# Kernel optimization log

Hardware: AMD Instinct MI355X
Metric: run time of the kernel (lower is better)

Reference implementation:

```python
import jax, jax.numpy as jnp
import numpy as np

N_HEAD, MODEL_DIM, KEY_DIM, VALUE_DIM = 16, 1024, 64, 64
B, S = 4, 2048
EPS = 1e-5
TEMP = float(np.sqrt(KEY_DIM))


def setup_inputs() -> dict:
    key = jax.random.key(0)
    ks = jax.random.split(key, 12)
    d = {
        'query': jax.random.normal(ks[0], (B, S, MODEL_DIM), jnp.float32),
        'key':   jax.random.normal(ks[1], (B, S, MODEL_DIM), jnp.float32),
        'value': jax.random.normal(ks[2], (B, S, MODEL_DIM), jnp.float32),
        # projection weights stored as [in, out]
        'Wq': jax.random.normal(ks[3], (MODEL_DIM, N_HEAD * KEY_DIM), jnp.float32) * np.sqrt(2.0 / (MODEL_DIM + KEY_DIM)),
        'bq': jnp.zeros((N_HEAD * KEY_DIM,), jnp.float32),
        'Wk': jax.random.normal(ks[4], (MODEL_DIM, N_HEAD * KEY_DIM), jnp.float32) * np.sqrt(2.0 / (MODEL_DIM + KEY_DIM)),
        'bk': jnp.zeros((N_HEAD * KEY_DIM,), jnp.float32),
        'Wv': jax.random.normal(ks[5], (MODEL_DIM, N_HEAD * VALUE_DIM), jnp.float32) * np.sqrt(2.0 / (MODEL_DIM + VALUE_DIM)),
        'bv': jnp.zeros((N_HEAD * VALUE_DIM,), jnp.float32),
        'Wo': jax.random.normal(ks[6], (N_HEAD * VALUE_DIM, MODEL_DIM), jnp.float32) * np.sqrt(2.0 / (N_HEAD * VALUE_DIM + MODEL_DIM)),
        'bo': jnp.zeros((MODEL_DIM,), jnp.float32),
        'ln_gamma': jnp.ones((MODEL_DIM,), jnp.float32),
        'ln_beta': jnp.zeros((MODEL_DIM,), jnp.float32),
    }
    return d


def reference(query, key, value, Wq, bq, Wk, bk, Wv, bv, Wo, bo, ln_gamma, ln_beta):
    b, sq, _ = query.shape
    residual = query
    # QKV projections -> [B, S, H, D]
    q = (query @ Wq + bq).reshape(b, sq, N_HEAD, KEY_DIM)
    k = (key @ Wk + bk).reshape(b, key.shape[1], N_HEAD, KEY_DIM)
    v = (value @ Wv + bv).reshape(b, value.shape[1], N_HEAD, VALUE_DIM)
    # scaled dot-product attention (dropout inactive in eval)
    scores = jnp.einsum('bqhd,bkhd->bhqk', q, k) / TEMP
    attn = jax.nn.softmax(scores, axis=-1)
    out = jnp.einsum('bhqk,bkhd->bqhd', attn, v).reshape(b, sq, N_HEAD * VALUE_DIM)
    # output projection + residual + LayerNorm
    out = out @ Wo + bo + residual
    mu = jnp.mean(out, axis=-1, keepdims=True)
    var = jnp.var(out, axis=-1, keepdims=True)
    return (out - mu) * jax.lax.rsqrt(var + EPS) * ln_gamma + ln_beta
```

## Files before the change

### kernel.cpp

```cpp
#include <hip/hip_runtime.h>
#include <math.h>

#define MD 1024
#define NH 16
#define HD 64
#define BATCH 4
#define SEQ 2048

typedef __attribute__((ext_vector_type(8))) short short8;
typedef __attribute__((ext_vector_type(4))) short short4v;
typedef __attribute__((ext_vector_type(4))) float f32x4;
typedef __attribute__((ext_vector_type(2))) unsigned int uint2v;

#define GLOAD16(gp, lp) __builtin_amdgcn_global_load_lds( \
    (const __attribute__((address_space(1))) void*)(gp),  \
    (__attribute__((address_space(3))) void*)(lp), 16, 0, 0)

__device__ inline unsigned short f2b(float f) {
    unsigned u = __builtin_bit_cast(unsigned, f);
    unsigned r = (u + 0x7fffu + ((u >> 16) & 1u)) >> 16;
    return (unsigned short)r;
}
__device__ inline float b2f(unsigned short s) {
    return __builtin_bit_cast(float, ((unsigned)s) << 16);
}

__global__ __launch_bounds__(256)
void prep_kernel(const float* __restrict__ x0, const float* __restrict__ x1,
                 const float* __restrict__ x2, unsigned short* __restrict__ y0,
                 unsigned short* __restrict__ y1, unsigned short* __restrict__ y2,
                 int n,
                 const float* __restrict__ W0, const float* __restrict__ W1,
                 const float* __restrict__ W2, const float* __restrict__ W3,
                 unsigned short* __restrict__ T0, unsigned short* __restrict__ T1,
                 unsigned short* __restrict__ T2, unsigned short* __restrict__ T3)
{
    __shared__ __attribute__((aligned(16))) float T[64][68];
    const int tid = threadIdx.x;
    if (blockIdx.y < 3) {
        const float* x = (blockIdx.y == 0) ? x0 : (blockIdx.y == 1) ? x1 : x2;
        unsigned short* y = (blockIdx.y == 0) ? y0 : (blockIdx.y == 1) ? y1 : y2;
        int i = (blockIdx.x * 256 + tid) * 8;
        if (i >= n) return;
        f32x4 a = *(const f32x4*)(x + i);
        f32x4 b = *(const f32x4*)(x + i + 4);
        short8 o;
        o[0] = (short)f2b(a[0]); o[1] = (short)f2b(a[1]);
        o[2] = (short)f2b(a[2]); o[3] = (short)f2b(a[3]);
        o[4] = (short)f2b(b[0]); o[5] = (short)f2b(b[1]);
        o[6] = (short)f2b(b[2]); o[7] = (short)f2b(b[3]);
        *(short8*)(y + i) = o;
        return;
    }
    const int bx = blockIdx.x;
    if (bx >= 1024) return;
    const int z = bx >> 8, t = bx & 255;
    const int nt = t & 15, kt = t >> 4;
    const float* W = (z == 0) ? W0 : (z == 1) ? W1 : (z == 2) ? W2 : W3;
    unsigned short* WT = (z == 0) ? T0 : (z == 1) ? T1 : (z == 2) ? T2 : T3;
    #pragma unroll
    for (int i = 0; i < 4; ++i) {
        int u = tid + i * 256;
        int row = u >> 4, c4 = u & 15;
        f32x4 v = *(const f32x4*)(W + (size_t)(kt * 64 + row) * MD + nt * 64 + c4 * 4);
        *(f32x4*)&T[row][c4 * 4] = v;
    }
    __syncthreads();
    #pragma unroll
    for (int i = 0; i < 2; ++i) {
        int u = tid + i * 256;
        int nn = u >> 3, c16 = u & 7;
        short8 o;
        #pragma unroll
        for (int j = 0; j < 8; ++j) o[j] = (short)f2b(T[c16 * 8 + j][nn]);
        *(short8*)(WT + (size_t)(nt * 64 + nn) * MD + kt * 64 + c16 * 8) = o;
    }
}

__device__ __forceinline__ void tile_origin(int* obrow, int* obcol)
{
    const int nbx = gridDim.x;
    const int bid = blockIdx.y * nbx + blockIdx.x;
    const int cpx = (nbx * gridDim.y) >> 3;
    const int swz = (bid & 7) * cpx + (bid >> 3);
    *obrow = (swz / nbx) * 128;
    *obcol = (swz % nbx) * 128;
}

__device__ __forceinline__
void gemm_core3(const unsigned short* __restrict__ A,
                const unsigned short* __restrict__ Bt,
                short* As, short* Bs, f32x4 acc[4][4],
                int brow, int bcol)
{
    const int tid = threadIdx.x;
    const int lane = tid & 63;
    const int wave = tid >> 6;
    const int wm = wave >> 1, wn = wave & 1;
    const int l15 = lane & 15, g = lane >> 4;

    #pragma unroll
    for (int m = 0; m < 4; ++m)
        #pragma unroll
        for (int n = 0; n < 4; ++n) acc[m][n] = (f32x4){0.f, 0.f, 0.f, 0.f};

    const int rA = tid >> 2, cA = (tid & 3) * 8;
    const int rB = rA + 64;

    auto stage = [&](int t) {
        const int kb = t << 5;
        short* as = As + (t % 3) * 4096;
        short* bs = Bs + (t % 3) * 4096;
        GLOAD16(A  + (size_t)(brow + rA) * MD + kb + cA, as + tid * 8);
        GLOAD16(A  + (size_t)(brow + rB) * MD + kb + cA, as + (tid + 256) * 8);
        GLOAD16(Bt + (size_t)(bcol + rA) * MD + kb + cA, bs + tid * 8);
        GLOAD16(Bt + (size_t)(bcol + rB) * MD + kb + cA, bs + (tid + 256) * 8);
    };

    stage(0);
    stage(1);

    for (int t = 0; t < 31; ++t) {
        asm volatile("s_waitcnt vmcnt(4)" ::: "memory");
        __builtin_amdgcn_s_barrier();
        __builtin_amdgcn_sched_barrier(0);
        if (t < 30) stage(t + 2);
        const short* as = As + (t % 3) * 4096;
        const short* bs = Bs + (t % 3) * 4096;
        short8 af[4], bf_[4];
        #pragma unroll
        for (int m = 0; m < 4; ++m)
            af[m] = *(const short8*)&as[(wm * 64 + m * 16 + l15) * 32 + g * 8];
        #pragma unroll
        for (int n = 0; n < 4; ++n)
            bf_[n] = *(const short8*)&bs[(wn * 64 + n * 16 + l15) * 32 + g * 8];
        #pragma unroll
        for (int m = 0; m < 4; ++m)
            #pragma unroll
            for (int n = 0; n < 4; ++n)
                acc[m][n] = __builtin_amdgcn_mfma_f32_16x16x32_bf16(af[m], bf_[n], acc[m][n], 0, 0, 0);
    }
    {
        asm volatile("s_waitcnt vmcnt(0)" ::: "memory");
        __builtin_amdgcn_s_barrier();
        __builtin_amdgcn_sched_barrier(0);
        const short* as = As + (31 % 3) * 4096;
        const short* bs = Bs + (31 % 3) * 4096;
        short8 af[4], bf_[4];
        #pragma unroll
        for (int m = 0; m < 4; ++m)
            af[m] = *(const short8*)&as[(wm * 64 + m * 16 + l15) * 32 + g * 8];
        #pragma unroll
        for (int n = 0; n < 4; ++n)
            bf_[n] = *(const short8*)&bs[(wn * 64 + n * 16 + l15) * 32 + g * 8];
        #pragma unroll
        for (int m = 0; m < 4; ++m)
            #pragma unroll
            for (int n = 0; n < 4; ++n)
                acc[m][n] = __builtin_amdgcn_mfma_f32_16x16x32_bf16(af[m], bf_[n], acc[m][n], 0, 0, 0);
    }
}

__global__ __launch_bounds__(256, 2)
void gemm_qkv(const unsigned short* __restrict__ A0, const unsigned short* __restrict__ A1,
              const unsigned short* __restrict__ A2,
              const unsigned short* __restrict__ B0, const unsigned short* __restrict__ B1,
              const unsigned short* __restrict__ B2,
              const float* __restrict__ b0, const float* __restrict__ b1,
              const float* __restrict__ b2,
              unsigned short* __restrict__ Cq, unsigned short* __restrict__ Ck,
              unsigned short* __restrict__ Cvt)
{
    __shared__ __attribute__((aligned(16))) short As[3 * 4096];
    __shared__ __attribute__((aligned(16))) short Bs[3 * 4096];
    const int z = blockIdx.z;
    const unsigned short* A  = (z == 0) ? A0 : (z == 1) ? A1 : A2;
    const unsigned short* Bt = (z == 0) ? B0 : (z == 1) ? B1 : B2;
    const float* bias        = (z == 0) ? b0 : (z == 1) ? b1 : b2;

    int brow, bcol;
    tile_origin(&brow, &bcol);
    f32x4 acc[4][4];
    gemm_core3(A, Bt, As, Bs, acc, brow, bcol);

    const int tid = threadIdx.x;
    const int lane = tid & 63;
    const int wave = tid >> 6;
    const int wm = wave >> 1, wn = wave & 1;
    const int l15 = lane & 15, g = lane >> 4;

    if (z == 2) {
        #pragma unroll
        for (int m = 0; m < 4; ++m) {
            #pragma unroll
            for (int n = 0; n < 4; ++n) {
                const int col = bcol + wn * 64 + n * 16 + l15;
                const int h = col >> 6, d = col & 63;
                const float bv_ = bias[col];
                const int row0 = brow + wm * 64 + m * 16 + 4 * g;
                const int bb = row0 >> 11, s = row0 & 2047;
                short4v pk;
                #pragma unroll
                for (int r = 0; r < 4; ++r) pk[r] = (short)f2b(acc[m][n][r] + bv_);
                *(short4v*)(Cvt + ((size_t)((bb << 4) + h) * 64 + d) * SEQ + s) = pk;
            }
        }
        return;
    }
    const float scale = (z == 0) ? (0.125f * 1.44269504088896f) : 1.0f;
    unsigned short* C = (z == 0) ? Cq : Ck;
    #pragma unroll
    for (int m = 0; m < 4; ++m) {
        #pragma unroll
        for (int n = 0; n < 4; ++n) {
            const int col = bcol + wn * 64 + n * 16 + l15;
            const float bcol_v = bias[col];
            #pragma unroll
            for (int r = 0; r < 4; ++r) {
                const size_t row = (size_t)(brow + wm * 64 + m * 16 + 4 * g + r);
                C[row * MD + col] = f2b((acc[m][n][r] + bcol_v) * scale);
            }
        }
    }
}

__global__ __launch_bounds__(256, 2)
void gemm_o(const unsigned short* __restrict__ A, const unsigned short* __restrict__ Bt,
            const float* __restrict__ bias, const float* __restrict__ residual,
            float* __restrict__ Cf)
{
    __shared__ __attribute__((aligned(16))) short As[3 * 4096];
    __shared__ __attribute__((aligned(16))) short Bs[3 * 4096];
    int brow, bcol;
    tile_origin(&brow, &bcol);
    f32x4 acc[4][4];
    gemm_core3(A, Bt, As, Bs, acc, brow, bcol);

    const int tid = threadIdx.x;
    const int lane = tid & 63;
    const int wave = tid >> 6;
    const int wm = wave >> 1, wn = wave & 1;
    const int l15 = lane & 15, g = lane >> 4;
    #pragma unroll
    for (int m = 0; m < 4; ++m) {
        #pragma unroll
        for (int n = 0; n < 4; ++n) {
            const int col = bcol + wn * 64 + n * 16 + l15;
            const float bcol_v = bias[col];
            #pragma unroll
            for (int r = 0; r < 4; ++r) {
                const size_t row = (size_t)(brow + wm * 64 + m * 16 + 4 * g + r);
                Cf[row * MD + col] = acc[m][n][r] + bcol_v + residual[row * MD + col];
            }
        }
    }
}

__global__ __launch_bounds__(256, 2)
void attn_mfma(const unsigned short* __restrict__ qp,
               const unsigned short* __restrict__ kp,
               const unsigned short* __restrict__ vt,
               unsigned short* __restrict__ ao)
{
    __shared__ __attribute__((aligned(16))) short Ps[256 * 64];
    __shared__ __attribute__((aligned(16))) short Ks[2][64 * 64];
    __shared__ __attribute__((aligned(16))) short Vts[2][64 * 64];

    const int tid = threadIdx.x;
    const int lane = tid & 63;
    const int wave = tid >> 6;
    const int l15 = lane & 15, g = lane >> 4;

    const int lin = blockIdx.y * gridDim.x + blockIdx.x;
    const int xi = lin & 7, j = lin >> 3;
    const int bh = xi + 8 * (j & 7);
    const int qt = j >> 3;

    const int b = bh >> 4, h = bh & 15;
    const size_t rowbase = (size_t)b * SEQ;
    const int q0 = qt * 256;
    const int wq = wave * 64;
    const int NT = SEQ / 64;

    const int r0 = tid >> 3, c16 = tid & 7;
    const int r1 = r0 + 32;
    const int lds0 = (r0 * 8 + (c16 ^ (r0 & 7))) * 8;
    const int lds1 = (r1 * 8 + (c16 ^ (r1 & 7))) * 8;
    const unsigned short* kbase = kp + (rowbase + r0) * MD + h * 64 + c16 * 8;
    const unsigned short* vbase = vt + ((size_t)bh * 64 + r0) * SEQ + c16 * 8;

    short8 qreg[4][2];
    #pragma unroll
    for (int nf = 0; nf < 4; ++nf)
        #pragma unroll
        for (int ki = 0; ki < 2; ++ki)
            qreg[nf][ki] = *(const short8*)(qp + (rowbase + q0 + wq + nf * 16 + l15) * MD
                                               + h * 64 + ki * 32 + g * 8);

    {
        short8 k0v = *(const short8*)(kbase);
        short8 k1v = *(const short8*)(kbase + 32 * MD);
        short8 v0v = *(const short8*)(vbase);
        short8 v1v = *(const short8*)(vbase + 32 * SEQ);
        *(short8*)&Ks[0][lds0]  = k0v;
        *(short8*)&Ks[0][lds1]  = k1v;
        *(short8*)&Vts[0][lds0] = v0v;
        *(short8*)&Vts[0][lds1] = v1v;
    }
    __syncthreads();

    short8 ones;
    #pragma unroll
    for (int jj = 0; jj < 8; ++jj) ones[jj] = (short)0x3F80;

    float mrun[4] = {-INFINITY, -INFINITY, -INFINITY, -INFINITY};
    f32x4 lrun[4];
    f32x4 off[4][4];
    #pragma unroll
    for (int qf = 0; qf < 4; ++qf) {
        lrun[qf] = (f32x4){0.f, 0.f, 0.f, 0.f};
        #pragma unroll
        for (int df = 0; df < 4; ++df) off[qf][df] = (f32x4){0.f, 0.f, 0.f, 0.f};
    }

    for (int kt = 0; kt < NT; ++kt) {
        const int cur = kt & 1;

        short8 kreg0, kreg1, vreg0, vreg1;
        if (kt + 1 < NT) {
            const unsigned short* kb = kbase + (size_t)(kt + 1) * 64 * MD;
            const unsigned short* vb = vbase + (kt + 1) * 64;
            kreg0 = *(const short8*)(kb);
            kreg1 = *(const short8*)(kb + 32 * MD);
            vreg0 = *(const short8*)(vb);
            vreg1 = *(const short8*)(vb + 32 * SEQ);
        }

        f32x4 sc[4][4];
        #pragma unroll
        for (int mf = 0; mf < 4; ++mf)
            #pragma unroll
            for (int nf = 0; nf < 4; ++nf) sc[mf][nf] = (f32x4){0.f, 0.f, 0.f, 0.f};
        __builtin_amdgcn_s_setprio(1);
        #pragma unroll
        for (int ki = 0; ki < 2; ++ki) {
            const int cu = ki * 4 + g;
            short8 af[4];
            #pragma unroll
            for (int mf = 0; mf < 4; ++mf) {
                int row = mf * 16 + l15;
                af[mf] = *(const short8*)&Ks[cur][(row * 8 + (cu ^ (row & 7))) * 8];
            }
            #pragma unroll
            for (int mf = 0; mf < 4; ++mf)
                #pragma unroll
                for (int nf = 0; nf < 4; ++nf)
                    sc[mf][nf] = __builtin_amdgcn_mfma_f32_16x16x32_bf16(af[mf], qreg[nf][ki], sc[mf][nf], 0, 0, 0);
        }
        __builtin_amdgcn_s_setprio(0);

        float pmax[4];
        #pragma unroll
        for (int nf = 0; nf < 4; ++nf) {
            float pm = fmaxf(fmaxf(sc[0][nf][0], sc[0][nf][1]), sc[0][nf][2]);
            pm = fmaxf(fmaxf(pm, sc[0][nf][3]), sc[1][nf][0]);
            pm = fmaxf(fmaxf(pm, sc[1][nf][1]), sc[1][nf][2]);
            pm = fmaxf(fmaxf(pm, sc[1][nf][3]), sc[2][nf][0]);
            pm = fmaxf(fmaxf(pm, sc[2][nf][1]), sc[2][nf][2]);
            pm = fmaxf(fmaxf(pm, sc[2][nf][3]), sc[3][nf][0]);
            pm = fmaxf(fmaxf(pm, sc[3][nf][1]), sc[3][nf][2]);
            pm = fmaxf(pm, sc[3][nf][3]);
            pm = fmaxf(pm, __shfl_xor(pm, 16));
            pm = fmaxf(pm, __shfl_xor(pm, 32));
            pmax[nf] = pm;
        }
        const int defer = (pmax[0] <= mrun[0] + 8.0f) && (pmax[1] <= mrun[1] + 8.0f) &&
                          (pmax[2] <= mrun[2] + 8.0f) && (pmax[3] <= mrun[3] + 8.0f);
        if (!__all(defer)) {
            float corr[4];
            #pragma unroll
            for (int nf = 0; nf < 4; ++nf) {
                float mnew = fmaxf(mrun[nf], pmax[nf]);
                corr[nf] = __builtin_amdgcn_exp2f(mrun[nf] - mnew);
                mrun[nf] = mnew;
            }
            #pragma unroll
            for (int qf = 0; qf < 4; ++qf)
                #pragma unroll
                for (int r = 0; r < 4; ++r) {
                    float c = __shfl(corr[qf], 4 * g + r);
                    lrun[qf][r] *= c;
                    #pragma unroll
                    for (int df = 0; df < 4; ++df) off[qf][df][r] *= c;
                }
        }
        #pragma unroll
        for (int nf = 0; nf < 4; ++nf) {
            const float nm = mrun[nf];
            #pragma unroll
            for (int mf = 0; mf < 4; ++mf)
                #pragma unroll
                for (int r = 0; r < 4; ++r)
                    sc[mf][nf][r] = __builtin_amdgcn_exp2f(sc[mf][nf][r] - nm);
        }

        #pragma unroll
        for (int nf = 0; nf < 4; ++nf) {
            int row = wq + nf * 16 + l15;
            #pragma unroll
            for (int mf = 0; mf < 4; ++mf) {
                unsigned p01, p23;
                asm("v_cvt_pk_bf16_f32 %0, %1, %2" : "=v"(p01) : "v"(sc[mf][nf][0]), "v"(sc[mf][nf][1]));
                asm("v_cvt_pk_bf16_f32 %0, %1, %2" : "=v"(p23) : "v"(sc[mf][nf][2]), "v"(sc[mf][nf][3]));
                uint2v pk = {p01, p23};
                int su = (mf * 2 + (g >> 1)) ^ (row & 7);
                *(uint2v*)&Ps[row * 64 + su * 8 + (g & 1) * 4] = pk;
            }
        }

        f32x4 ts[4];
        #pragma unroll
        for (int qf = 0; qf < 4; ++qf) ts[qf] = (f32x4){0.f, 0.f, 0.f, 0.f};
        __builtin_amdgcn_s_setprio(1);
        #pragma unroll
        for (int ki = 0; ki < 2; ++ki) {
            const int cu = ki * 4 + g;
            short8 pa[4], vb[4];
            #pragma unroll
            for (int qf = 0; qf < 4; ++qf) {
                int row = wq + qf * 16 + l15;
                pa[qf] = *(const short8*)&Ps[(row * 8 + (cu ^ (row & 7))) * 8];
            }
            #pragma unroll
            for (int df = 0; df < 4; ++df) {
                int d = df * 16 + l15;
                vb[df] = *(const short8*)&Vts[cur][(d * 8 + (cu ^ (d & 7))) * 8];
            }
            #pragma unroll
            for (int qf = 0; qf < 4; ++qf)
                #pragma unroll
                for (int df = 0; df < 4; ++df)
                    off[qf][df] = __builtin_amdgcn_mfma_f32_16x16x32_bf16(pa[qf], vb[df], off[qf][df], 0, 0, 0);
            #pragma unroll
            for (int qf = 0; qf < 4; ++qf)
                ts[qf] = __builtin_amdgcn_mfma_f32_16x16x32_bf16(pa[qf], ones, ts[qf], 0, 0, 0);
        }
        __builtin_amdgcn_s_setprio(0);
        #pragma unroll
        for (int qf = 0; qf < 4; ++qf)
            #pragma unroll
            for (int r = 0; r < 4; ++r) lrun[qf][r] += ts[qf][r];

        if (kt + 1 < NT) {
            const int nxt = cur ^ 1;
            *(short8*)&Ks[nxt][lds0]  = kreg0;
            *(short8*)&Ks[nxt][lds1]  = kreg1;
            *(short8*)&Vts[nxt][lds0] = vreg0;
            *(short8*)&Vts[nxt][lds1] = vreg1;
        }
        __syncthreads();
    }

    #pragma unroll
    for (int qf = 0; qf < 4; ++qf) {
        #pragma unroll
        for (int r = 0; r < 4; ++r) {
            const float inv = 1.0f / lrun[qf][r];
            const size_t row = rowbase + q0 + wq + qf * 16 + 4 * g + r;
            #pragma unroll
            for (int df = 0; df < 4; ++df) {
                float val = off[qf][df][r] * inv;
                ao[row * MD + h * 64 + df * 16 + l15] = f2b(val);
            }
        }
    }
}

__global__ __launch_bounds__(256)
void ln_kernel(float* __restrict__ X, const float* __restrict__ gamma,
               const float* __restrict__ beta)
{
    const int row = blockIdx.x;
    const int tid = threadIdx.x;
    float* px = X + (size_t)row * MD;
    f32x4 x = ((const f32x4*)px)[tid];
    float s  = x[0] + x[1] + x[2] + x[3];
    float ss = fmaf(x[0], x[0], fmaf(x[1], x[1], fmaf(x[2], x[2], x[3] * x[3])));
    #pragma unroll
    for (int off = 1; off < 64; off <<= 1) {
        s  += __shfl_xor(s,  off);
        ss += __shfl_xor(ss, off);
    }
    __shared__ float red[8];
    const int wid = tid >> 6;
    if ((tid & 63) == 0) { red[wid] = s; red[wid + 4] = ss; }
    __syncthreads();
    s  = red[0] + red[1] + red[2] + red[3];
    ss = red[4] + red[5] + red[6] + red[7];
    const float mu   = s * (1.0f / MD);
    const float var  = ss * (1.0f / MD) - mu * mu;
    const float rstd = rsqrtf(var + 1e-5f);
    f32x4 gm = ((const f32x4*)gamma)[tid];
    f32x4 be = ((const f32x4*)beta)[tid];
    f32x4 r;
    r[0] = (x[0] - mu) * rstd * gm[0] + be[0];
    r[1] = (x[1] - mu) * rstd * gm[1] + be[1];
    r[2] = (x[2] - mu) * rstd * gm[2] + be[2];
    r[3] = (x[3] - mu) * rstd * gm[3] + be[3];
    ((f32x4*)px)[tid] = r;
}

extern "C" void kernel_launch(void* const* d_in, const int* in_sizes, int n_in,
                              void* d_out, int out_size, void* d_ws, size_t ws_size,
                              hipStream_t stream)
{
    const float* query = (const float*)d_in[0];
    const float* key   = (const float*)d_in[1];
    const float* value = (const float*)d_in[2];
    const float* Wq = (const float*)d_in[3];
    const float* bq = (const float*)d_in[4];
    const float* Wk = (const float*)d_in[5];
    const float* bk = (const float*)d_in[6];
    const float* Wv = (const float*)d_in[7];
    const float* bv = (const float*)d_in[8];
    const float* Wo = (const float*)d_in[9];
    const float* bo = (const float*)d_in[10];
    const float* gamma = (const float*)d_in[11];
    const float* beta  = (const float*)d_in[12];
    float* out = (float*)d_out;

    const size_t NTOK = (size_t)BATCH * SEQ;
    const size_t ACT  = NTOK * MD;

    unsigned short* qa  = (unsigned short*)d_ws;
    unsigned short* ka  = qa + ACT;
    unsigned short* va  = ka + ACT;
    unsigned short* WqT = va + ACT;
    unsigned short* WkT = WqT + (size_t)MD * MD;
    unsigned short* WvT = WkT + (size_t)MD * MD;
    unsigned short* WoT = WvT + (size_t)MD * MD;
    unsigned short* qp  = WoT + (size_t)MD * MD;
    unsigned short* kp  = qp + ACT;
    unsigned short* vtp = kp + ACT;
    unsigned short* ao  = ka;

    dim3 blk(256);

    prep_kernel<<<dim3(4096, 4), blk, 0, stream>>>(
        query, key, value, qa, ka, va, (int)ACT,
        Wq, Wk, Wv, Wo, WqT, WkT, WvT, WoT);

    dim3 gg(MD / 128, NTOK / 128, 3);
    gemm_qkv<<<gg, blk, 0, stream>>>(qa, ka, va, WqT, WkT, WvT,
                                     bq, bk, bv, qp, kp, vtp);

    attn_mfma<<<dim3(SEQ / 256, 64), blk, 0, stream>>>(qp, kp, vtp, ao);

    gemm_o<<<dim3(MD / 128, NTOK / 128), blk, 0, stream>>>(ao, WoT, bo, query, out);

    ln_kernel<<<NTOK, blk, 0, stream>>>(out, gamma, beta);
}
```

Baseline: 219.3 us.

## Fuse fp32-to-bf16 activation conversion into QKV GEMM A-tile loads

Result: slower. 224.7 us (+2.4%).

```diff
diff --git a/kernel.cpp b/kernel.cpp
--- a/kernel.cpp
+++ b/kernel.cpp
@@ -11,6 +11,7 @@
 typedef __attribute__((ext_vector_type(4))) short short4v;
 typedef __attribute__((ext_vector_type(4))) float f32x4;
 typedef __attribute__((ext_vector_type(2))) unsigned int uint2v;
+typedef __attribute__((ext_vector_type(4))) unsigned int uint4v;
 
 #define GLOAD16(gp, lp) __builtin_amdgcn_global_load_lds( \
     (const __attribute__((address_space(1))) void*)(gp),  \
@@ -21,39 +22,16 @@
     unsigned r = (u + 0x7fffu + ((u >> 16) & 1u)) >> 16;
     return (unsigned short)r;
 }
-__device__ inline float b2f(unsigned short s) {
-    return __builtin_bit_cast(float, ((unsigned)s) << 16);
-}
 
 __global__ __launch_bounds__(256)
-void prep_kernel(const float* __restrict__ x0, const float* __restrict__ x1,
-                 const float* __restrict__ x2, unsigned short* __restrict__ y0,
-                 unsigned short* __restrict__ y1, unsigned short* __restrict__ y2,
-                 int n,
-                 const float* __restrict__ W0, const float* __restrict__ W1,
-                 const float* __restrict__ W2, const float* __restrict__ W3,
-                 unsigned short* __restrict__ T0, unsigned short* __restrict__ T1,
-                 unsigned short* __restrict__ T2, unsigned short* __restrict__ T3)
+void wtrans4(const float* __restrict__ W0, const float* __restrict__ W1,
+             const float* __restrict__ W2, const float* __restrict__ W3,
+             unsigned short* __restrict__ T0, unsigned short* __restrict__ T1,
+             unsigned short* __restrict__ T2, unsigned short* __restrict__ T3)
 {
     __shared__ __attribute__((aligned(16))) float T[64][68];
     const int tid = threadIdx.x;
-    if (blockIdx.y < 3) {
-        const float* x = (blockIdx.y == 0) ? x0 : (blockIdx.y == 1) ? x1 : x2;
-        unsigned short* y = (blockIdx.y == 0) ? y0 : (blockIdx.y == 1) ? y1 : y2;
-        int i = (blockIdx.x * 256 + tid) * 8;
-        if (i >= n) return;
-        f32x4 a = *(const f32x4*)(x + i);
-        f32x4 b = *(const f32x4*)(x + i + 4);
-        short8 o;
-        o[0] = (short)f2b(a[0]); o[1] = (short)f2b(a[1]);
-        o[2] = (short)f2b(a[2]); o[3] = (short)f2b(a[3]);
-        o[4] = (short)f2b(b[0]); o[5] = (short)f2b(b[1]);
-        o[6] = (short)f2b(b[2]); o[7] = (short)f2b(b[3]);
-        *(short8*)(y + i) = o;
-        return;
-    }
     const int bx = blockIdx.x;
-    if (bx >= 1024) return;
     const int z = bx >> 8, t = bx & 255;
     const int nt = t & 15, kt = t >> 4;
     const float* W = (z == 0) ? W0 : (z == 1) ? W1 : (z == 2) ? W2 : W3;
@@ -88,10 +66,10 @@
 }
 
 __device__ __forceinline__
-void gemm_core3(const unsigned short* __restrict__ A,
-                const unsigned short* __restrict__ Bt,
-                short* As, short* Bs, f32x4 acc[4][4],
-                int brow, int bcol)
+void gemm_core3_f32(const float* __restrict__ A,
+                    const unsigned short* __restrict__ Bt,
+                    float* As32, short* Bs, f32x4 acc[4][4],
+                    int brow, int bcol)
 {
     const int tid = threadIdx.x;
     const int lane = tid & 63;
@@ -104,33 +82,48 @@
         #pragma unroll
         for (int n = 0; n < 4; ++n) acc[m][n] = (f32x4){0.f, 0.f, 0.f, 0.f};
 
-    const int rA = tid >> 2, cA = (tid & 3) * 8;
-    const int rB = rA + 64;
+    const int rB = tid >> 2, cB = (tid & 3) * 8;
+    const int rB2 = rB + 64;
 
     auto stage = [&](int t) {
         const int kb = t << 5;
-        short* as = As + (t % 3) * 4096;
+        float* as = As32 + (t % 3) * 4096;
         short* bs = Bs + (t % 3) * 4096;
-        GLOAD16(A  + (size_t)(brow + rA) * MD + kb + cA, as + tid * 8);
-        GLOAD16(A  + (size_t)(brow + rB) * MD + kb + cA, as + (tid + 256) * 8);
-        GLOAD16(Bt + (size_t)(bcol + rA) * MD + kb + cA, bs + tid * 8);
-        GLOAD16(Bt + (size_t)(bcol + rB) * MD + kb + cA, bs + (tid + 256) * 8);
+        #pragma unroll
+        for (int i = 0; i < 4; ++i) {
+            const int U = i * 256 + tid;
+            const int row = U >> 3, cu = U & 7;
+            const int cs = cu ^ ((row & 3) << 1);
+            GLOAD16(A + (size_t)(brow + row) * MD + kb + cs * 4, as + U * 4);
+        }
+        GLOAD16(Bt + (size_t)(bcol + rB)  * MD + kb + cB, bs + tid * 8);
+        GLOAD16(Bt + (size_t)(bcol + rB2) * MD + kb + cB, bs + (tid + 256) * 8);
     };
 
     stage(0);
     stage(1);
 
     for (int t = 0; t < 31; ++t) {
-        asm volatile("s_waitcnt vmcnt(4)" ::: "memory");
+        asm volatile("s_waitcnt vmcnt(6)" ::: "memory");
         __builtin_amdgcn_s_barrier();
         __builtin_amdgcn_sched_barrier(0);
         if (t < 30) stage(t + 2);
-        const short* as = As + (t % 3) * 4096;
+        const float* as = As32 + (t % 3) * 4096;
         const short* bs = Bs + (t % 3) * 4096;
         short8 af[4], bf_[4];
         #pragma unroll
-        for (int m = 0; m < 4; ++m)
-            af[m] = *(const short8*)&as[(wm * 64 + m * 16 + l15) * 32 + g * 8];
+        for (int m = 0; m < 4; ++m) {
+            const int row = wm * 64 + m * 16 + l15;
+            const int u0 = row * 8 + ((g * 2) ^ ((row & 3) << 1));
+            f32x4 a0 = *(const f32x4*)&as[u0 * 4];
+            f32x4 a1 = *(const f32x4*)&as[(u0 + 1) * 4];
+            unsigned w0, w1, w2, w3;
+            asm("v_cvt_pk_bf16_f32 %0, %1, %2" : "=v"(w0) : "v"(a0[0]), "v"(a0[1]));
+            asm("v_cvt_pk_bf16_f32 %0, %1, %2" : "=v"(w1) : "v"(a0[2]), "v"(a0[3]));
+            asm("v_cvt_pk_bf16_f32 %0, %1, %2" : "=v"(w2) : "v"(a1[0]), "v"(a1[1]));
+            asm("v_cvt_pk_bf16_f32 %0, %1, %2" : "=v"(w3) : "v"(a1[2]), "v"(a1[3]));
+            af[m] = __builtin_bit_cast(short8, (uint4v){w0, w1, w2, w3});
+        }
         #pragma unroll
         for (int n = 0; n < 4; ++n)
             bf_[n] = *(const short8*)&bs[(wn * 64 + n * 16 + l15) * 32 + g * 8];
@@ -144,12 +137,22 @@
         asm volatile("s_waitcnt vmcnt(0)" ::: "memory");
         __builtin_amdgcn_s_barrier();
         __builtin_amdgcn_sched_barrier(0);
-        const short* as = As + (31 % 3) * 4096;
+        const float* as = As32 + (31 % 3) * 4096;
         const short* bs = Bs + (31 % 3) * 4096;
         short8 af[4], bf_[4];
         #pragma unroll
-        for (int m = 0; m < 4; ++m)
-            af[m] = *(const short8*)&as[(wm * 64 + m * 16 + l15) * 32 + g * 8];
+        for (int m = 0; m < 4; ++m) {
+            const int row = wm * 64 + m * 16 + l15;
+            const int u0 = row * 8 + ((g * 2) ^ ((row & 3) << 1));
+            f32x4 a0 = *(const f32x4*)&as[u0 * 4];
+            f32x4 a1 = *(const f32x4*)&as[(u0 + 1) * 4];
+            unsigned w0, w1, w2, w3;
+            asm("v_cvt_pk_bf16_f32 %0, %1, %2" : "=v"(w0) : "v"(a0[0]), "v"(a0[1]));
+            asm("v_cvt_pk_bf16_f32 %0, %1, %2" : "=v"(w1) : "v"(a0[2]), "v"(a0[3]));
+            asm("v_cvt_pk_bf16_f32 %0, %1, %2" : "=v"(w2) : "v"(a1[0]), "v"(a1[1]));
+            asm("v_cvt_pk_bf16_f32 %0, %1, %2" : "=v"(w3) : "v"(a1[2]), "v"(a1[3]));
+            af[m] = __builtin_bit_cast(short8, (uint4v){w0, w1, w2, w3});
+        }
         #pragma unroll
         for (int n = 0; n < 4; ++n)
             bf_[n] = *(const short8*)&bs[(wn * 64 + n * 16 + l15) * 32 + g * 8];
@@ -162,8 +165,8 @@
 }
 
 __global__ __launch_bounds__(256, 2)
-void gemm_qkv(const unsigned short* __restrict__ A0, const unsigned short* __restrict__ A1,
-              const unsigned short* __restrict__ A2,
+void gemm_qkv(const float* __restrict__ A0, const float* __restrict__ A1,
+              const float* __restrict__ A2,
               const unsigned short* __restrict__ B0, const unsigned short* __restrict__ B1,
               const unsigned short* __restrict__ B2,
               const float* __restrict__ b0, const float* __restrict__ b1,
@@ -171,17 +174,17 @@
               unsigned short* __restrict__ Cq, unsigned short* __restrict__ Ck,
               unsigned short* __restrict__ Cvt)
 {
-    __shared__ __attribute__((aligned(16))) short As[3 * 4096];
+    __shared__ __attribute__((aligned(16))) float As32[3 * 4096];
     __shared__ __attribute__((aligned(16))) short Bs[3 * 4096];
     const int z = blockIdx.z;
-    const unsigned short* A  = (z == 0) ? A0 : (z == 1) ? A1 : A2;
+    const float* A           = (z == 0) ? A0 : (z == 1) ? A1 : A2;
     const unsigned short* Bt = (z == 0) ? B0 : (z == 1) ? B1 : B2;
     const float* bias        = (z == 0) ? b0 : (z == 1) ? b1 : b2;
 
     int brow, bcol;
     tile_origin(&brow, &bcol);
     f32x4 acc[4][4];
-    gemm_core3(A, Bt, As, Bs, acc, brow, bcol);
+    gemm_core3_f32(A, Bt, As32, Bs, acc, brow, bcol);
 
     const int tid = threadIdx.x;
     const int lane = tid & 63;
@@ -221,6 +224,80 @@
                 C[row * MD + col] = f2b((acc[m][n][r] + bcol_v) * scale);
             }
         }
+    }
+}
+
+__device__ __forceinline__
+void gemm_core3(const unsigned short* __restrict__ A,
+                const unsigned short* __restrict__ Bt,
+                short* As, short* Bs, f32x4 acc[4][4],
+                int brow, int bcol)
+{
+    const int tid = threadIdx.x;
+    const int lane = tid & 63;
+    const int wave = tid >> 6;
+    const int wm = wave >> 1, wn = wave & 1;
+    const int l15 = lane & 15, g = lane >> 4;
+
+    #pragma unroll
+    for (int m = 0; m < 4; ++m)
+        #pragma unroll
+        for (int n = 0; n < 4; ++n) acc[m][n] = (f32x4){0.f, 0.f, 0.f, 0.f};
+
+    const int rA = tid >> 2, cA = (tid & 3) * 8;
+    const int rB = rA + 64;
+
+    auto stage = [&](int t) {
+        const int kb = t << 5;
+        short* as = As + (t % 3) * 4096;
+        short* bs = Bs + (t % 3) * 4096;
+        GLOAD16(A  + (size_t)(brow + rA) * MD + kb + cA, as + tid * 8);
+        GLOAD16(A  + (size_t)(brow + rB) * MD + kb + cA, as + (tid + 256) * 8);
+        GLOAD16(Bt + (size_t)(bcol + rA) * MD + kb + cA, bs + tid * 8);
+        GLOAD16(Bt + (size_t)(bcol + rB) * MD + kb + cA, bs + (tid + 256) * 8);
+    };
+
+    stage(0);
+    stage(1);
+
+    for (int t = 0; t < 31; ++t) {
+        asm volatile("s_waitcnt vmcnt(4)" ::: "memory");
+        __builtin_amdgcn_s_barrier();
+        __builtin_amdgcn_sched_barrier(0);
+        if (t < 30) stage(t + 2);
+        const short* as = As + (t % 3) * 4096;
+        const short* bs = Bs + (t % 3) * 4096;
+        short8 af[4], bf_[4];
+        #pragma unroll
+        for (int m = 0; m < 4; ++m)
+            af[m] = *(const short8*)&as[(wm * 64 + m * 16 + l15) * 32 + g * 8];
+        #pragma unroll
+        for (int n = 0; n < 4; ++n)
+            bf_[n] = *(const short8*)&bs[(wn * 64 + n * 16 + l15) * 32 + g * 8];
+        #pragma unroll
+        for (int m = 0; m < 4; ++m)
+            #pragma unroll
+            for (int n = 0; n < 4; ++n)
+                acc[m][n] = __builtin_amdgcn_mfma_f32_16x16x32_bf16(af[m], bf_[n], acc[m][n], 0, 0, 0);
+    }
+    {
+        asm volatile("s_waitcnt vmcnt(0)" ::: "memory");
+        __builtin_amdgcn_s_barrier();
+        __builtin_amdgcn_sched_barrier(0);
+        const short* as = As + (31 % 3) * 4096;
+        const short* bs = Bs + (31 % 3) * 4096;
+        short8 af[4], bf_[4];
+        #pragma unroll
+        for (int m = 0; m < 4; ++m)
+            af[m] = *(const short8*)&as[(wm * 64 + m * 16 + l15) * 32 + g * 8];
+        #pragma unroll
+        for (int n = 0; n < 4; ++n)
+            bf_[n] = *(const short8*)&bs[(wn * 64 + n * 16 + l15) * 32 + g * 8];
+        #pragma unroll
+        for (int m = 0; m < 4; ++m)
+            #pragma unroll
+            for (int n = 0; n < 4; ++n)
+                acc[m][n] = __builtin_amdgcn_mfma_f32_16x16x32_bf16(af[m], bf_[n], acc[m][n], 0, 0, 0);
     }
 }
 
@@ -532,26 +609,21 @@
     const size_t NTOK = (size_t)BATCH * SEQ;
     const size_t ACT  = NTOK * MD;
 
-    unsigned short* qa  = (unsigned short*)d_ws;
-    unsigned short* ka  = qa + ACT;
-    unsigned short* va  = ka + ACT;
-    unsigned short* WqT = va + ACT;
+    unsigned short* WqT = (unsigned short*)d_ws;
     unsigned short* WkT = WqT + (size_t)MD * MD;
     unsigned short* WvT = WkT + (size_t)MD * MD;
     unsigned short* WoT = WvT + (size_t)MD * MD;
     unsigned short* qp  = WoT + (size_t)MD * MD;
     unsigned short* kp  = qp + ACT;
     unsigned short* vtp = kp + ACT;
-    unsigned short* ao  = ka;
+    unsigned short* ao  = vtp + ACT;
 
     dim3 blk(256);
 
-    prep_kernel<<<dim3(4096, 4), blk, 0, stream>>>(
-        query, key, value, qa, ka, va, (int)ACT,
-        Wq, Wk, Wv, Wo, WqT, WkT, WvT, WoT);
+    wtrans4<<<1024, blk, 0, stream>>>(Wq, Wk, Wv, Wo, WqT, WkT, WvT, WoT);
 
     dim3 gg(MD / 128, NTOK / 128, 3);
-    gemm_qkv<<<gg, blk, 0, stream>>>(qa, ka, va, WqT, WkT, WvT,
+    gemm_qkv<<<gg, blk, 0, stream>>>(query, key, value, WqT, WkT, WvT,
                                      bq, bk, bv, qp, kp, vtp);
 
     attn_mfma<<<dim3(SEQ / 256, 64), blk, 0, stream>>>(qp, kp, vtp, ao);
```
